# Kernel optimization log

Hardware: AMD Instinct MI355X
Metric: run time of the kernel (lower is better)

The kernel has to match this reference:

```python
import jax, jax.numpy as jnp
import numpy as np

B, R, C, D = 8, 64, 16, 128  # batch, num_rows(taxa), patch_num, embed_dim


def _linear_init(key, fan_in, fan_out):
    lim = 1.0 / np.sqrt(fan_in)
    kw, kb = jax.random.split(key)
    W = jax.random.uniform(kw, (fan_in, fan_out), jnp.float32, -lim, lim)
    b = jax.random.uniform(kb, (fan_out,), jnp.float32, -lim, lim)
    return W, b


def setup_inputs() -> dict:
    key = jax.random.key(0)
    ks = jax.random.split(key, 8)
    row_np, col_np = np.triu_indices(R, k=1)  # n = R*(R-1)/2 = 2016 pairs
    hW, hb = _linear_init(ks[1], D, D)
    gW, gb = _linear_init(ks[2], D, D)
    qW, qb = _linear_init(ks[3], D, D)
    kW, kb = _linear_init(ks[4], D, D)
    s1W, s1b = _linear_init(ks[5], D, D)
    s2W, s2b = _linear_init(ks[6], D, 1)
    return {
        "batch_input": jax.random.normal(ks[0], (B, R, C, D), jnp.float32),
        "seq_mask": jnp.ones((B, 1, C), jnp.float32),
        "row": jnp.asarray(row_np, jnp.int32),
        "col": jnp.asarray(col_np, jnp.int32),
        "hW": hW, "hb": hb, "gW": gW, "gb": gb,
        "qW": qW, "qb": qb, "kW": kW, "kb": kb,
        "s1W": s1W, "s1b": s1b, "s2W": s2W, "s2b": s2b,
    }


def reference(batch_input, seq_mask, row, col,
              hW, hb, gW, gb, qW, qb, kW, kb, s1W, s1b, s2W, s2b):
    b, r, c, d = batch_input.shape
    n = row.shape[0]
    # pairwise gather: x_i, x_j -> [b, n, c, d]
    x_i = batch_input[:, row]
    x_j = batch_input[:, col]
    # sigmoid gate fusion of the pair
    h = (x_i - x_j) @ hW + hb
    z = jax.nn.sigmoid(h)
    x = z * x_i + (1.0 - z) * x_j
    # masked global attention over the batch_input 'memory' (r > 2 branch)
    q = x @ qW + qb                    # [b, n, c, d]
    k = batch_input @ kW + kb          # [b, r, c, d]
    scale = 1.0 / np.sqrt(d * c).astype(np.float32)
    alpha = jnp.einsum('bncd,brcd->bnr', q, k) * scale
    # -inf at (pair n, rows row[n] and col[n]); equivalent to += -inf on finite scores
    neg_mask = (jnp.zeros((n, r), bool)
                .at[jnp.arange(n), row].set(True)
                .at[jnp.arange(n), col].set(True))
    alpha = jnp.where(neg_mask[None], -jnp.inf, alpha)
    alpha = jax.nn.softmax(alpha, axis=-1)
    x_glob = jnp.einsum('bnr,brcd->bncd', alpha, batch_input)
    g = x_glob @ gW + gb
    w = jax.nn.sigmoid(g)
    x = (1.0 - w) * x + w * x_glob
    # s_out: Linear -> GELU(exact) -> Linear(d,1), then mask and reduce over c
    s = jax.nn.gelu(x @ s1W + s1b, approximate=False) @ s2W + s2b  # [b, n, c, 1]
    scores = s[..., 0] * seq_mask       # seq_mask [b,1,c] broadcasts over n
    return scores.sum(-1)               # [b, n]
```

## Files before the change

kernel.cpp:

```cpp
#include <hip/hip_runtime.h>
#include <hip/hip_bf16.h>
#include <math.h>

#define B_    8
#define R_    64
#define C_    16
#define D_    128
#define NPAIR 2016
#define CD    2048
#define PG    32
#define NPG   63
#define XSTR  136
#define LSTR  68
#define NEG_BIG (-1e30f)
#define SCALE 0.022097086912079608f

typedef __attribute__((ext_vector_type(8))) short short8;
typedef __attribute__((ext_vector_type(4))) float float4v;

#define WMH  0u
#define WML  16384u
#define WSH  98304u
#define VECO 131072u
#define QBKO 131592u
#define MO   132616u
#define XTO  1181192u
#define GTO  2229768u
#define HO   3278344u

__device__ __forceinline__ unsigned short f2b(float f){
    union { float f; unsigned int u; } v; v.f = f;
    const unsigned int r = v.u + 0x7FFFu + ((v.u >> 16) & 1u);
    return (unsigned short)(r >> 16);
}
__device__ __forceinline__ float b2f(unsigned short u){
    union { unsigned int i; float f; } v; v.i = ((unsigned int)u) << 16; return v.f;
}
__device__ __forceinline__ float lo2f(unsigned int u){
    union { unsigned int i; float f; } v; v.i = u << 16; return v.f;
}
__device__ __forceinline__ float hif2f(unsigned int u){
    union { unsigned int i; float f; } v; v.i = u & 0xffff0000u; return v.f;
}
__device__ __forceinline__ unsigned int pack2(float a, float b){
    unsigned int r;
    asm("v_cvt_pk_bf16_f32 %0, %1, %2" : "=v"(r) : "v"(a), "v"(b));
    return r;
}
__device__ __forceinline__ unsigned short f2b1(float a){
    unsigned int r;
    asm("v_cvt_pk_bf16_f32 %0, %1, %1" : "=v"(r) : "v"(a));
    return (unsigned short)r;
}
__device__ __forceinline__ void split_bf(float v, float* hi, float* lo){
    union { float f; unsigned int u; } x; x.f = v;
    const unsigned int r = (x.u + 0x7FFFu + ((x.u >> 16) & 1u)) & 0xffff0000u;
    union { unsigned int u; float f; } h; h.u = r;
    *hi = h.f; *lo = v - h.f;
}
__device__ __forceinline__ void splitw(float v, short* h, short* l){
    union { float f; unsigned int u; } x; x.f = v;
    const unsigned int rh = (x.u + 0x7FFFu + ((x.u >> 16) & 1u)) & 0xffff0000u;
    union { unsigned int u; float f; } hf; hf.u = rh;
    *h = (short)(rh >> 16);
    *l = (short)f2b(v - hf.f);
}
__device__ __forceinline__ float sigmoid_safe(float x){
    return __builtin_amdgcn_rcpf(1.f + __expf(-x));
}
__device__ __forceinline__ float gelu_tanh(float x){
    const float u = x*x;
    const float g2 = x*(1.5957691216057308f + 0.07135481627159f*u);
    return x * sigmoid_safe(g2);
}

__global__ __launch_bounds__(256) void k_prepA(
    const float* __restrict__ qW, const float* __restrict__ qb,
    const float* __restrict__ kW, const float* __restrict__ kb,
    unsigned short* __restrict__ ws)
{
    const int bid = blockIdx.x, t = threadIdx.x;
    if (bid < 64){
        __shared__ float sKW[2][128];
        const int e0 = bid*2;
        sKW[t>>7][t&127] = kW[(e0 + (t>>7))*128 + (t&127)];
        __syncthreads();
        const int e = t>>7, d = t&127;
        const float* qr = qW + d*128;
        const float* kr = sKW[e];
        float acc = 0.f;
        #pragma unroll 8
        for (int g = 0; g < 128; g += 4){
            const float4 qv = *reinterpret_cast<const float4*>(qr + g);
            acc += qv.x*kr[g] + qv.y*kr[g+1] + qv.z*kr[g+2] + qv.w*kr[g+3];
        }
        float hi, lo; split_bf(acc, &hi, &lo);
        ws[WMH + d*128 + (e0+e)] = f2b(hi);
        ws[WML + d*128 + (e0+e)] = f2b(lo);
    } else {
        float* vec = (float*)(ws + VECO);
        if (t < 128){
            float a1 = 0.f, a2 = 0.f;
            #pragma unroll 8
            for (int g = 0; g < 128; g += 4){
                const float4 q4 = *reinterpret_cast<const float4*>(qW + t*128 + g);
                const float4 k4 = *reinterpret_cast<const float4*>(kW + t*128 + g);
                const float4 kb4 = *reinterpret_cast<const float4*>(kb + g);
                const float4 qb4 = *reinterpret_cast<const float4*>(qb + g);
                a1 += q4.x*kb4.x + q4.y*kb4.y + q4.z*kb4.z + q4.w*kb4.w;
                a2 += k4.x*qb4.x + k4.y*qb4.y + k4.z*qb4.z + k4.w*qb4.w;
            }
            vec[t] = a1;
            vec[128 + t] = a2;
        } else if (t == 128){
            float a = 0.f;
            for (int g = 0; g < 128; ++g) a = fmaf(qb[g], kb[g], a);
            vec[256] = a;
        }
    }
}

__global__ __launch_bounds__(512) void k_prepB(const float* __restrict__ x,
        const float* __restrict__ hW, const float* __restrict__ gW,
        const float* __restrict__ gb, const float* __restrict__ s1W,
        unsigned short* __restrict__ ws)
{
    __shared__ __align__(16) unsigned short smem[8832];
    __shared__ float sQ[4];
    const int bid = blockIdx.x, t = threadIdx.x;
    const int w = t >> 6, lane = t & 63, l15 = lane & 15, quad = lane >> 4;

    if (bid < 128){
        unsigned short* sH = smem;
        const int br0 = bid * 4;
        const float* kqf = (const float*)(ws + VECO) + 128;
        const float* mbf = (const float*)(ws + VECO);
        if (t < 4) sQ[t] = 0.f;
        __syncthreads();
        float qacc[4] = {0.f, 0.f, 0.f, 0.f};
        #pragma unroll
        for (int i = 0; i < 4; ++i){
            const int flat = (t + 512*i)*4;
            const int lr = i;
            const int cd = flat & 2047;
            const float4 v = *reinterpret_cast<const float4*>(x + (size_t)(br0+lr)*CD + cd);
            const int ad = (lr*16 + (cd>>7))*XSTR + lr*8 + (cd & 127);
            uint2 uh;
            uh.x = pack2(v.x, v.y); uh.y = pack2(v.z, v.w);
            *reinterpret_cast<uint2*>(sH + ad) = uh;
            const float4 kq4 = *reinterpret_cast<const float4*>(kqf + (cd & 127));
            qacc[i] = v.x*kq4.x + v.y*kq4.y + v.z*kq4.z + v.w*kq4.w;
        }
        #pragma unroll
        for (int i = 0; i < 4; ++i){
            float s = qacc[i];
            #pragma unroll
            for (int off = 1; off < 64; off <<= 1) s += __shfl_xor(s, off);
            if (lane == 0) atomicAdd(&sQ[i], s);
        }
        __syncthreads();
        {
            const float bv = mbf[w*16 + l15];
            float4v acc[4];
            #pragma unroll
            for (int mt = 0; mt < 4; ++mt){ float4v d = {bv,bv,bv,bv}; acc[mt] = d; }
            #pragma unroll
            for (int ks = 0; ks < 4; ++ks){
                const int ko = ks*32 + quad*8;
                const int bd = (w*16 + l15)*128 + ko;
                const short8 bh = *reinterpret_cast<const short8*>(ws + WMH + bd);
                const short8 bl = *reinterpret_cast<const short8*>(ws + WML + bd);
                #pragma unroll
                for (int mt = 0; mt < 4; ++mt){
                    const int ad = (mt*16 + l15)*XSTR + mt*8 + ko;
                    const short8 ah = *reinterpret_cast<const short8*>(sH + ad);
                    float4v d = acc[mt];
                    d = __builtin_amdgcn_mfma_f32_16x16x32_bf16(ah, bh, d, 0,0,0);
                    d = __builtin_amdgcn_mfma_f32_16x16x32_bf16(ah, bl, d, 0,0,0);
                    acc[mt] = d;
                }
            }
            const int f = w*16 + l15;
            #pragma unroll
            for (int mt = 0; mt < 4; ++mt)
            #pragma unroll
            for (int e = 0; e < 4; ++e){
                const int c = quad*4 + e;
                ws[MO + (size_t)(br0+mt)*CD + c*128 + f] = f2b(acc[mt][e]);
            }
            if (t < 4){
                const float s0 = ((const float*)(ws + VECO))[256];
                ((float*)(ws + QBKO))[br0 + t] = sQ[t] + 16.f*s0;
            }
        }
        {
            const int n = w*16 + l15;
            float4v acc[4];
            #pragma unroll
            for (int mt = 0; mt < 4; ++mt){ float4v z = {0.f,0.f,0.f,0.f}; acc[mt] = z; }
            #pragma unroll
            for (int ks = 0; ks < 4; ++ks){
                const int ko = ks*32 + quad*8;
                short8 bh, bl;
                #pragma unroll
                for (int j = 0; j < 8; ++j){
                    short hh, ll;
                    splitw(hW[(size_t)(ko+j)*128 + n], &hh, &ll);
                    bh[j] = hh; bl[j] = ll;
                }
                #pragma unroll
                for (int mt = 0; mt < 4; ++mt){
                    const int ad = (mt*16 + l15)*XSTR + mt*8 + ko;
                    const short8 ah = *reinterpret_cast<const short8*>(sH + ad);
                    float4v d = acc[mt];
                    d = __builtin_amdgcn_mfma_f32_16x16x32_bf16(ah, bh, d, 0,0,0);
                    d = __builtin_amdgcn_mfma_f32_16x16x32_bf16(ah, bl, d, 0,0,0);
                    acc[mt] = d;
                }
            }
            #pragma unroll
            for (int mt = 0; mt < 4; ++mt)
            #pragma unroll
            for (int e = 0; e < 4; ++e){
                const int c = quad*4 + e;
                ws[HO + (size_t)(br0+mt)*CD + c*128 + n] = f2b(acc[mt][e]);
            }
        }
    } else if (bid < 256){
        unsigned short* tileB = smem;
        const int gidx = bid - 128;
        const int b = gidx >> 4, cd0 = (gidx & 15)*128;
        #pragma unroll
        for (int i = 0; i < 16; ++i){
            const int idx = i*512 + t;
            const int r = idx >> 7, dd = idx & 127;
            tileB[r*138 + dd] = f2b(x[(size_t)(b*64 + r)*CD + cd0 + dd]);
        }
        __syncthreads();
        {
            const unsigned int base = XTO + (unsigned int)(b*2048 + cd0)*64;
            #pragma unroll
            for (int j = 0; j < 16; ++j){
                const int idx = j*512 + t;
                const int cc = idx >> 6, r = idx & 63;
                ws[base + cc*64 + r] = tileB[r*138 + cc];
            }
        }
        const int fA = w*16 + l15;
        float4v acc[4];
        #pragma unroll
        for (int nt = 0; nt < 4; ++nt){ float4v z = {0.f,0.f,0.f,0.f}; acc[nt] = z; }
        #pragma unroll
        for (int ks = 0; ks < 4; ++ks){
            const int ko = ks*32 + quad*8;
            short8 ah, al;
            #pragma unroll
            for (int j = 0; j < 8; ++j){
                short hh, ll;
                splitw(gW[(size_t)(ko+j)*128 + fA], &hh, &ll);
                ah[j] = hh; al[j] = ll;
            }
            #pragma unroll
            for (int nt = 0; nt < 4; ++nt){
                const short8 bb = *reinterpret_cast<const short8*>(tileB + (nt*16 + l15)*138 + ko);
                float4v d = acc[nt];
                d = __builtin_amdgcn_mfma_f32_16x16x32_bf16(ah, bb, d, 0,0,0);
                d = __builtin_amdgcn_mfma_f32_16x16x32_bf16(al, bb, d, 0,0,0);
                acc[nt] = d;
            }
        }
        #pragma unroll
        for (int nt = 0; nt < 4; ++nt)
        #pragma unroll
        for (int e = 0; e < 4; ++e){
            const int f = w*16 + quad*4 + e;
            const float val = acc[nt][e] + gb[f];
            ws[GTO + (size_t)(b*2048 + cd0 + f)*64 + nt*16 + l15] = f2b(val);
        }
    } else {
        const int gid = (bid - 256)*4096 + t;
        #pragma unroll
        for (int i = 0; i < 8; ++i){
            const int g = gid + i*512;
            const int n = g >> 7, k = g & 127;
            ws[WSH + g] = f2b(s1W[k*128 + n]);
        }
    }
}

__global__ __launch_bounds__(1024, 4) void k_main(
    const float* __restrict__ x, const float* __restrict__ seq_mask,
    const int* __restrict__ row, const int* __restrict__ col,
    const float* __restrict__ hb, const float* __restrict__ s1b,
    const float* __restrict__ s2W, const float* __restrict__ s2b,
    const unsigned short* __restrict__ ws, float* __restrict__ out)
{
    __shared__ __align__(16) unsigned short sX[512*XSTR + 256];
    __shared__ __align__(16) unsigned short sAl[32*72];
    __shared__ float sLog[32*LSTR];
    __shared__ float sOut[PG];
    __shared__ float sMask[16];
    __shared__ int srp[PG], scp[PG];

    const int t = threadIdx.x;
    const int w = t >> 6, lane = t & 63, l15 = lane & 15, quad = lane >> 4;
    const int b = blockIdx.x, p0 = blockIdx.y * PG;
    const float* xb = x + (size_t)b * R_ * CD;
    const unsigned short* Hb = ws + HO + (size_t)b * R_ * CD;

    const int rt = w & 3, kh = w >> 2;
    const int r2 = rt*16 + l15;
    const unsigned short* Mr = ws + MO + ((size_t)b*64 + r2)*CD + kh*512;
    short8 bhr0[8];
    #pragma unroll
    for (int u = 0; u < 8; ++u)
        bhr0[u] = *reinterpret_cast<const short8*>(Mr + u*32 + quad*8);

    if (t < PG){ srp[t] = row[p0+t]; scp[t] = col[p0+t]; sOut[t] = 0.f; }
    if (t >= 32 && t < 48) sMask[t-32] = seq_mask[b*C_ + (t-32)];
    for (int i = t; i < 32*LSTR; i += 1024) sLog[i] = 0.f;
    __syncthreads();

    #pragma unroll
    for (int i = 0; i < 8; ++i){
        const int flat = (t + 1024*i)*8;
        const int p = flat >> 11, cd = flat & 2047;
        const int ri = srp[p], ci = scp[p];
        const float* xip = xb + (size_t)ri*CD + cd;
        const float* xjp = xb + (size_t)ci*CD + cd;
        const float4 xi0 = *reinterpret_cast<const float4*>(xip);
        const float4 xi1 = *reinterpret_cast<const float4*>(xip + 4);
        const float4 xj0 = *reinterpret_cast<const float4*>(xjp);
        const float4 xj1 = *reinterpret_cast<const float4*>(xjp + 4);
        const uint4 Hi4 = *reinterpret_cast<const uint4*>(Hb + (size_t)ri*CD + cd);
        const uint4 Hj4 = *reinterpret_cast<const uint4*>(Hb + (size_t)ci*CD + cd);
        const float4 h40 = *reinterpret_cast<const float4*>(hb + (cd & 127));
        const float4 h41 = *reinterpret_cast<const float4*>(hb + (cd & 127) + 4);
        const float z0 = sigmoid_safe(lo2f(Hi4.x)  - lo2f(Hj4.x)  + h40.x);
        const float z1 = sigmoid_safe(hif2f(Hi4.x) - hif2f(Hj4.x) + h40.y);
        const float z2 = sigmoid_safe(lo2f(Hi4.y)  - lo2f(Hj4.y)  + h40.z);
        const float z3 = sigmoid_safe(hif2f(Hi4.y) - hif2f(Hj4.y) + h40.w);
        const float z4 = sigmoid_safe(lo2f(Hi4.z)  - lo2f(Hj4.z)  + h41.x);
        const float z5 = sigmoid_safe(hif2f(Hi4.z) - hif2f(Hj4.z) + h41.y);
        const float z6 = sigmoid_safe(lo2f(Hi4.w)  - lo2f(Hj4.w)  + h41.z);
        const float z7 = sigmoid_safe(hif2f(Hi4.w) - hif2f(Hj4.w) + h41.w);
        const float v0 = xj0.x + z0*(xi0.x - xj0.x);
        const float v1 = xj0.y + z1*(xi0.y - xj0.y);
        const float v2 = xj0.z + z2*(xi0.z - xj0.z);
        const float v3 = xj0.w + z3*(xi0.w - xj0.w);
        const float v4 = xj1.x + z4*(xi1.x - xj1.x);
        const float v5 = xj1.y + z5*(xi1.y - xj1.y);
        const float v6 = xj1.z + z6*(xi1.z - xj1.z);
        const float v7 = xj1.w + z7*(xi1.w - xj1.w);
        const int ad = (p*16 + (cd>>7))*XSTR + p*8 + (cd & 127);
        uint4 uv;
        uv.x = pack2(v0,v1); uv.y = pack2(v2,v3);
        uv.z = pack2(v4,v5); uv.w = pack2(v6,v7);
        *reinterpret_cast<uint4*>(sX + ad) = uv;
    }
    __syncthreads();

    const unsigned short* XTb = ws + XTO + (size_t)b * CD * 64;
    const unsigned short* GTb = ws + GTO + (size_t)b * CD * 64;
    short8 px0[2], px1[2], pg0[2], pg1[2];

    {
        short8 bhr1[8];
        #pragma unroll
        for (int u = 0; u < 8; ++u)
            bhr1[u] = *reinterpret_cast<const short8*>(Mr + (8+u)*32 + quad*8);
        float4v d0a = {0.f,0.f,0.f,0.f}, d0b = {0.f,0.f,0.f,0.f};
        float4v d1a = {0.f,0.f,0.f,0.f}, d1b = {0.f,0.f,0.f,0.f};
        #pragma unroll
        for (int u = 0; u < 8; ++u){
            const int k = kh*512 + u*32 + quad*8;
            const int khi = k >> 7, klo = k & 127;
            const short8 ahA = *reinterpret_cast<const short8*>(
                sX + (l15*16 + khi)*XSTR + l15*8 + klo);
            const short8 ahB = *reinterpret_cast<const short8*>(
                sX + ((16+l15)*16 + khi)*XSTR + (16+l15)*8 + klo);
            if (u & 1){
                d0b = __builtin_amdgcn_mfma_f32_16x16x32_bf16(ahA, bhr0[u], d0b, 0,0,0);
                d1b = __builtin_amdgcn_mfma_f32_16x16x32_bf16(ahB, bhr0[u], d1b, 0,0,0);
            } else {
                d0a = __builtin_amdgcn_mfma_f32_16x16x32_bf16(ahA, bhr0[u], d0a, 0,0,0);
                d1a = __builtin_amdgcn_mfma_f32_16x16x32_bf16(ahB, bhr0[u], d1a, 0,0,0);
            }
        }
        #pragma unroll
        for (int j = 0; j < 2; ++j){
            const int cd = w*128 + j*16 + l15;
            px0[j] = *reinterpret_cast<const short8*>(XTb + (size_t)cd*64 + quad*8);
            px1[j] = *reinterpret_cast<const short8*>(XTb + (size_t)cd*64 + 32 + quad*8);
            pg0[j] = *reinterpret_cast<const short8*>(GTb + (size_t)cd*64 + quad*8);
            pg1[j] = *reinterpret_cast<const short8*>(GTb + (size_t)cd*64 + 32 + quad*8);
        }
        #pragma unroll
        for (int u = 0; u < 8; ++u){
            const int k = kh*512 + (8+u)*32 + quad*8;
            const int khi = k >> 7, klo = k & 127;
            const short8 ahA = *reinterpret_cast<const short8*>(
                sX + (l15*16 + khi)*XSTR + l15*8 + klo);
            const short8 ahB = *reinterpret_cast<const short8*>(
                sX + ((16+l15)*16 + khi)*XSTR + (16+l15)*8 + klo);
            if (u & 1){
                d0b = __builtin_amdgcn_mfma_f32_16x16x32_bf16(ahA, bhr1[u], d0b, 0,0,0);
                d1b = __builtin_amdgcn_mfma_f32_16x16x32_bf16(ahB, bhr1[u], d1b, 0,0,0);
            } else {
                d0a = __builtin_amdgcn_mfma_f32_16x16x32_bf16(ahA, bhr1[u], d0a, 0,0,0);
                d1a = __builtin_amdgcn_mfma_f32_16x16x32_bf16(ahB, bhr1[u], d1a, 0,0,0);
            }
        }
        const float4v dA = d0a + d0b;
        const float4v dB = d1a + d1b;
        #pragma unroll
        for (int e = 0; e < 4; ++e){
            const int pp = quad*4 + e;
            atomicAdd(&sLog[pp*LSTR + r2], dA[e]);
            atomicAdd(&sLog[(16+pp)*LSTR + r2], dB[e]);
        }
    }
    __syncthreads();

    if (t < 512){
        const int pp = t >> 4, l = t & 15;
        const int ri = srp[pp], ci = scp[pp];
        const float* qbk = (const float*)(ws + QBKO);
        float v[4]; float m = NEG_BIG;
        #pragma unroll
        for (int k = 0; k < 4; ++k){
            const int r = l + 16*k;
            float lv = (sLog[pp*LSTR + r] + qbk[b*64 + r]) * SCALE;
            if (r == ri || r == ci) lv = NEG_BIG;
            v[k] = lv; m = fmaxf(m, lv);
        }
        #pragma unroll
        for (int s = 1; s < 16; s <<= 1) m = fmaxf(m, __shfl_xor(m, s));
        float e4[4]; float sum = 0.f;
        #pragma unroll
        for (int k = 0; k < 4; ++k){
            const int r = l + 16*k;
            const bool masked = (r == ri || r == ci);
            const float e = masked ? 0.f : __expf(fmaxf(v[k]-m, -80.f));
            e4[k] = e; sum += e;
        }
        #pragma unroll
        for (int s = 1; s < 16; s <<= 1) sum += __shfl_xor(sum, s);
        const float inv = __builtin_amdgcn_rcpf(sum);
        #pragma unroll
        for (int k = 0; k < 4; ++k) sAl[pp*72 + l + 16*k] = f2b1(e4[k]*inv);
    }
    __syncthreads();

    const int mh = w >> 3, nw = w & 7;
    short8 bh4[4];
    #pragma unroll
    for (int ks = 0; ks < 4; ++ks)
        bh4[ks] = *reinterpret_cast<const short8*>(ws + WSH + (nw*16 + l15)*128 + ks*32 + quad*8);

    {
        const short8 AhA0 = *reinterpret_cast<const short8*>(sAl + l15*72 + quad*8);
        const short8 AhA1 = *reinterpret_cast<const short8*>(sAl + l15*72 + 32 + quad*8);
        const short8 AhB0 = *reinterpret_cast<const short8*>(sAl + (16+l15)*72 + quad*8);
        const short8 AhB1 = *reinterpret_cast<const short8*>(sAl + (16+l15)*72 + 32 + quad*8);
        #pragma unroll
        for (int j = 0; j < 8; ++j){
            const int s = j & 1;
            float4v dxA = {0.f,0.f,0.f,0.f}, dgA = {0.f,0.f,0.f,0.f};
            float4v dxB = {0.f,0.f,0.f,0.f}, dgB = {0.f,0.f,0.f,0.f};
            dxA = __builtin_amdgcn_mfma_f32_16x16x32_bf16(px0[s], AhA0, dxA, 0,0,0);
            dxA = __builtin_amdgcn_mfma_f32_16x16x32_bf16(px1[s], AhA1, dxA, 0,0,0);
            dgA = __builtin_amdgcn_mfma_f32_16x16x32_bf16(pg0[s], AhA0, dgA, 0,0,0);
            dgA = __builtin_amdgcn_mfma_f32_16x16x32_bf16(pg1[s], AhA1, dgA, 0,0,0);
            dxB = __builtin_amdgcn_mfma_f32_16x16x32_bf16(px0[s], AhB0, dxB, 0,0,0);
            dxB = __builtin_amdgcn_mfma_f32_16x16x32_bf16(px1[s], AhB1, dxB, 0,0,0);
            dgB = __builtin_amdgcn_mfma_f32_16x16x32_bf16(pg0[s], AhB0, dgB, 0,0,0);
            dgB = __builtin_amdgcn_mfma_f32_16x16x32_bf16(pg1[s], AhB1, dgB, 0,0,0);
            if (j + 2 < 8){
                const int cd2 = w*128 + (j+2)*16 + l15;
                px0[s] = *reinterpret_cast<const short8*>(XTb + (size_t)cd2*64 + quad*8);
                px1[s] = *reinterpret_cast<const short8*>(XTb + (size_t)cd2*64 + 32 + quad*8);
                pg0[s] = *reinterpret_cast<const short8*>(GTb + (size_t)cd2*64 + quad*8);
                pg1[s] = *reinterpret_cast<const short8*>(GTb + (size_t)cd2*64 + 32 + quad*8);
            }
            const int klo = j*16 + quad*4;
            {
                const int ad = (l15*16 + w)*XSTR + l15*8 + klo;
                uint2 xo = *reinterpret_cast<const uint2*>(sX + ad);
                const float o0 = lo2f(xo.x), o1 = hif2f(xo.x);
                const float o2 = lo2f(xo.y), o3 = hif2f(xo.y);
                const float w0 = sigmoid_safe(dgA[0]);
                const float w1 = sigmoid_safe(dgA[1]);
                const float w2 = sigmoid_safe(dgA[2]);
                const float w3 = sigmoid_safe(dgA[3]);
                const float n0 = (1.f - w0)*o0 + w0*dxA[0];
                const float n1 = (1.f - w1)*o1 + w1*dxA[1];
                const float n2 = (1.f - w2)*o2 + w2*dxA[2];
                const float n3 = (1.f - w3)*o3 + w3*dxA[3];
                uint2 nv; nv.x = pack2(n0, n1); nv.y = pack2(n2, n3);
                *reinterpret_cast<uint2*>(sX + ad) = nv;
            }
            {
                const int ad = ((16+l15)*16 + w)*XSTR + (16+l15)*8 + klo;
                uint2 xo = *reinterpret_cast<const uint2*>(sX + ad);
                const float o0 = lo2f(xo.x), o1 = hif2f(xo.x);
                const float o2 = lo2f(xo.y), o3 = hif2f(xo.y);
                const float w0 = sigmoid_safe(dgB[0]);
                const float w1 = sigmoid_safe(dgB[1]);
                const float w2 = sigmoid_safe(dgB[2]);
                const float w3 = sigmoid_safe(dgB[3]);
                const float n0 = (1.f - w0)*o0 + w0*dxB[0];
                const float n1 = (1.f - w1)*o1 + w1*dxB[1];
                const float n2 = (1.f - w2)*o2 + w2*dxB[2];
                const float n3 = (1.f - w3)*o3 + w3*dxB[3];
                uint2 nv; nv.x = pack2(n0, n1); nv.y = pack2(n2, n3);
                *reinterpret_cast<uint2*>(sX + ad) = nv;
            }
        }
    }
    __syncthreads();

    {
        float4v acc16[16];
        const float bv = s1b[nw*16 + l15];
        #pragma unroll
        for (int mt = 0; mt < 16; ++mt){ float4v d = {bv,bv,bv,bv}; acc16[mt] = d; }
        #pragma unroll
        for (int ks = 0; ks < 4; ++ks){
            const int ko = ks*32 + quad*8;
            #pragma unroll
            for (int mt = 0; mt < 16; ++mt){
                const int p = mh*16 + mt;
                const short8 a = *reinterpret_cast<const short8*>(sX + (p*16 + l15)*XSTR + p*8 + ko);
                acc16[mt] = __builtin_amdgcn_mfma_f32_16x16x32_bf16(a, bh4[ks], acc16[mt], 0,0,0);
            }
        }
        const float s2v = s2W[nw*16 + l15];
        const float mk0 = sMask[quad*4+0], mk1 = sMask[quad*4+1];
        const float mk2 = sMask[quad*4+2], mk3 = sMask[quad*4+3];
        float psum[16];
        #pragma unroll
        for (int mt = 0; mt < 16; ++mt){
            float s = gelu_tanh(acc16[mt][0]) * mk0;
            s += gelu_tanh(acc16[mt][1]) * mk1;
            s += gelu_tanh(acc16[mt][2]) * mk2;
            s += gelu_tanh(acc16[mt][3]) * mk3;
            psum[mt] = s * s2v;
        }
        #pragma unroll
        for (int s = 1; s < 64; s <<= 1)
            #pragma unroll
            for (int mt = 0; mt < 16; ++mt) psum[mt] += __shfl_xor(psum[mt], s);
        if (lane == 0){
            #pragma unroll
            for (int mt = 0; mt < 16; ++mt) atomicAdd(&sOut[mh*16 + mt], psum[mt]);
        }
    }
    __syncthreads();

    if (t < PG){
        float msum = 0.f;
        #pragma unroll
        for (int c = 0; c < 16; ++c) msum += sMask[c];
        out[(size_t)b*NPAIR + p0 + t] = sOut[t] + s2b[0]*msum;
    }
}

extern "C" void kernel_launch(void* const* d_in, const int* in_sizes, int n_in,
                              void* d_out, int out_size, void* d_ws, size_t ws_size,
                              hipStream_t stream)
{
    const float* x    = (const float*)d_in[0];
    const float* mask = (const float*)d_in[1];
    const int*   row  = (const int*)d_in[2];
    const int*   col  = (const int*)d_in[3];
    const float* hW  = (const float*)d_in[4];  const float* hb  = (const float*)d_in[5];
    const float* gW  = (const float*)d_in[6];  const float* gb  = (const float*)d_in[7];
    const float* qW  = (const float*)d_in[8];  const float* qb  = (const float*)d_in[9];
    const float* kW  = (const float*)d_in[10]; const float* kb  = (const float*)d_in[11];
    const float* s1W = (const float*)d_in[12]; const float* s1b = (const float*)d_in[13];
    const float* s2W = (const float*)d_in[14]; const float* s2b = (const float*)d_in[15];

    unsigned short* ws = (unsigned short*)d_ws;

    k_prepA<<<65, 256, 0, stream>>>(qW, qb, kW, kb, ws);
    k_prepB<<<260, 512, 0, stream>>>(x, hW, gW, gb, s1W, ws);
    k_main<<<dim3(B_, NPG), 1024, 0, stream>>>(x, mask, row, col,
                                               hb, s1b, s2W, s2b,
                                               ws, (float*)d_out);
}
```

Measured before the change: 196.0 us.

## Retile final s1 MLP GEMM into 4x4 register blocks with cheaper reduction

The final Linear+GELU stage is remapped from each wave owning 16 row tiles times one 16-column tile to each wave owning a 4x4 block of 16x16 tiles. A and B fragments are each reused four times, which cuts LDS and global fragment loads per MFMA. The cross-lane reduction is restructured from a full 6-step butterfly on 16 values to partial shuffles, a quad-based select, and a 4-step butterfly. This also means far fewer shared-memory atomics. It requires more B-weight loads per k-step from global/workspace memory, and the register-pressure pattern changes.

```diff
diff --git a/kernel.cpp b/kernel.cpp
--- a/kernel.cpp
+++ b/kernel.cpp
@@ -452,11 +452,15 @@
     }
     __syncthreads();
 
-    const int mh = w >> 3, nw = w & 7;
-    short8 bh4[4];
+    const int mg = w >> 1, ng = w & 1;
+    short8 bf0[4]; float s2vj[4], bvj[4];
     #pragma unroll
-    for (int ks = 0; ks < 4; ++ks)
-        bh4[ks] = *reinterpret_cast<const short8*>(ws + WSH + (nw*16 + l15)*128 + ks*32 + quad*8);
+    for (int j = 0; j < 4; ++j){
+        const int n0 = (ng*4 + j)*16 + l15;
+        bf0[j] = *reinterpret_cast<const short8*>(ws + WSH + n0*128 + quad*8);
+        s2vj[j] = s2W[n0];
+        bvj[j] = s1b[n0];
+    }
 
     {
         const short8 AhA0 = *reinterpret_cast<const short8*>(sAl + l15*72 + quad*8);
@@ -521,39 +525,69 @@
     __syncthreads();
 
     {
-        float4v acc16[16];
-        const float bv = s1b[nw*16 + l15];
-        #pragma unroll
-        for (int mt = 0; mt < 16; ++mt){ float4v d = {bv,bv,bv,bv}; acc16[mt] = d; }
+        float4v acc[4][4];
+        #pragma unroll
+        for (int i = 0; i < 4; ++i)
+        #pragma unroll
+        for (int j = 0; j < 4; ++j){
+            float4v d = {bvj[j], bvj[j], bvj[j], bvj[j]};
+            acc[i][j] = d;
+        }
         #pragma unroll
         for (int ks = 0; ks < 4; ++ks){
             const int ko = ks*32 + quad*8;
-            #pragma unroll
-            for (int mt = 0; mt < 16; ++mt){
-                const int p = mh*16 + mt;
-                const short8 a = *reinterpret_cast<const short8*>(sX + (p*16 + l15)*XSTR + p*8 + ko);
-                acc16[mt] = __builtin_amdgcn_mfma_f32_16x16x32_bf16(a, bh4[ks], acc16[mt], 0,0,0);
-            }
-        }
-        const float s2v = s2W[nw*16 + l15];
+            short8 bf[4];
+            #pragma unroll
+            for (int j = 0; j < 4; ++j)
+                bf[j] = (ks == 0) ? bf0[j]
+                      : *reinterpret_cast<const short8*>(ws + WSH + ((ng*4+j)*16 + l15)*128 + ko);
+            short8 af[4];
+            #pragma unroll
+            for (int i = 0; i < 4; ++i){
+                const int p = mg*4 + i;
+                af[i] = *reinterpret_cast<const short8*>(sX + (p*16 + l15)*XSTR + p*8 + ko);
+            }
+            #pragma unroll
+            for (int i = 0; i < 4; ++i)
+            #pragma unroll
+            for (int j = 0; j < 4; ++j)
+                acc[i][j] = __builtin_amdgcn_mfma_f32_16x16x32_bf16(af[i], bf[j], acc[i][j], 0,0,0);
+        }
         const float mk0 = sMask[quad*4+0], mk1 = sMask[quad*4+1];
         const float mk2 = sMask[quad*4+2], mk3 = sMask[quad*4+3];
-        float psum[16];
-        #pragma unroll
-        for (int mt = 0; mt < 16; ++mt){
-            float s = gelu_tanh(acc16[mt][0]) * mk0;
-            s += gelu_tanh(acc16[mt][1]) * mk1;
-            s += gelu_tanh(acc16[mt][2]) * mk2;
-            s += gelu_tanh(acc16[mt][3]) * mk3;
-            psum[mt] = s * s2v;
-        }
-        #pragma unroll
-        for (int s = 1; s < 64; s <<= 1)
-            #pragma unroll
-            for (int mt = 0; mt < 16; ++mt) psum[mt] += __shfl_xor(psum[mt], s);
-        if (lane == 0){
-            #pragma unroll
-            for (int mt = 0; mt < 16; ++mt) atomicAdd(&sOut[mh*16 + mt], psum[mt]);
+        float psum[4][4];
+        #pragma unroll
+        for (int i = 0; i < 4; ++i)
+        #pragma unroll
+        for (int j = 0; j < 4; ++j){
+            float s = gelu_tanh(acc[i][j][0]) * mk0;
+            s += gelu_tanh(acc[i][j][1]) * mk1;
+            s += gelu_tanh(acc[i][j][2]) * mk2;
+            s += gelu_tanh(acc[i][j][3]) * mk3;
+            psum[i][j] = s * s2vj[j];
+        }
+        #pragma unroll
+        for (int i = 0; i < 4; ++i)
+        #pragma unroll
+        for (int j = 0; j < 4; ++j){
+            float v = psum[i][j];
+            v += __shfl_xor(v, 16);
+            v += __shfl_xor(v, 32);
+            psum[i][j] = v;
+        }
+        float v4[4];
+        #pragma unroll
+        for (int j = 0; j < 4; ++j)
+            v4[j] = (quad == 0) ? psum[0][j]
+                  : (quad == 1) ? psum[1][j]
+                  : (quad == 2) ? psum[2][j] : psum[3][j];
+        #pragma unroll
+        for (int s = 1; s < 16; s <<= 1)
+            #pragma unroll
+            for (int j = 0; j < 4; ++j) v4[j] += __shfl_xor(v4[j], s);
+        if (l15 == 0){
+            const float tot = (v4[0] + v4[1]) + (v4[2] + v4[3]);
+            atomicAdd(&sOut[mg*4 + quad], tot);
         }
     }
     __syncthreads();
```

Result: slower. 201.9 us (+3.0%).
